# Kernel tuning notes

Measured on AMD Instinct MI355X. Metric: run time of the kernel, lower is better.

The kernel has to match this reference:

```python
import jax, jax.numpy as jnp
import numpy as np

C, N, D, DQ, K = 8, 16384, 1024, 128, 128  # clusters, patches/cluster, feat dim, q dim, top_k per cluster


def setup_inputs() -> dict:
    key = jax.random.key(0)
    ks = jax.random.split(key, 4)
    s = 0.02
    return {
        "cluster_features": jax.random.normal(ks[0], (C, N, D), jnp.float32),
        "key_feats": jax.random.normal(ks[1], (C, 1, D), jnp.float32),
        "Wq": jax.random.normal(ks[2], (D, DQ), jnp.float32) * s,
        "bq": jnp.zeros((DQ,), jnp.float32),
        "Wv": jax.random.normal(ks[3], (D, D), jnp.float32) * s,
        "bv": jnp.zeros((D,), jnp.float32),
    }


def _ranking_topk(feats, key_feat, Wq, bq, Wv, bv):
    # feats: [n, d], key_feat: [1, d]
    Q = feats @ Wq + bq                     # [n, DQ]
    qk = key_feat @ Wq + bq                 # [1, DQ]
    A = Q @ qk.T                            # [n, 1] attention scores
    A = jax.nn.softmax(A / jnp.sqrt(jnp.float32(DQ)), axis=0)
    top_vals, top_idx = jax.lax.top_k(A[:, 0], K)   # sorted descending, like torch.topk
    top_feats = feats[top_idx]              # [K, d] gather
    V = top_feats @ Wv + bv                 # value projection on gathered subset only
    A_ = jax.nn.softmax(top_vals[:, None] / jnp.sqrt(jnp.float32(D)), axis=0)  # [K, 1]
    fusion = (A_.T @ V)[0]                  # [d] fused weighted sum
    return top_feats, fusion


def reference(cluster_features, key_feats, Wq, bq, Wv, bv):
    top_feats, fusion = jax.vmap(
        lambda f, kf: _ranking_topk(f, kf, Wq, bq, Wv, bv)
    )(cluster_features, key_feats)
    # concat per-cluster selections; C*K == num_sample_feature so no padding branch
    selected_features = top_feats.reshape(C * K, D)
    cluster_fusion_feature = fusion         # [C, D]
    return selected_features, cluster_fusion_feature
```

## Files before the change

### kernel.cpp

```cpp
#include <hip/hip_runtime.h>

#define C_CLUST 8
#define N_PAT   16384
#define D_FEAT  1024
#define DQ_DIM  128
#define K_TOP   128

#define INV_S128 0.08838834764831844055
#define INV_S1024 0.03125

__device__ inline unsigned f2key(float f) {
    unsigned u = __float_as_uint(f);
    return (u & 0x80000000u) ? ~u : (u | 0x80000000u);
}
__device__ inline float key2f(unsigned k) {
    unsigned u = (k & 0x80000000u) ? (k ^ 0x80000000u) : ~k;
    return __uint_as_float(u);
}

__global__ __launch_bounds__(128) void qk_kernel(
    const float* __restrict__ key_feats,
    const float* __restrict__ Wq,
    double* __restrict__ qk_part)
{
    const int b = blockIdx.x;
    const int c = b >> 4, sg = b & 15;
    const int j = threadIdx.x;
    const int d0 = sg * 64;
    double acc = 0.0;
#pragma unroll 4
    for (int d = d0; d < d0 + 64; ++d)
        acc += (double)key_feats[c * D_FEAT + d] * (double)Wq[d * DQ_DIM + j];
    qk_part[(size_t)(c * 16 + sg) * DQ_DIM + j] = acc;
}

__global__ __launch_bounds__(256) void r_kernel(
    const float* __restrict__ Wq,
    const float* __restrict__ bq,
    const double* __restrict__ qk_part,
    double* __restrict__ r,
    double* __restrict__ b0)
{
    const int w = blockIdx.x * 4 + (threadIdx.x >> 6);
    const int lane = threadIdx.x & 63;
    const int c = w >> 10, d = w & (D_FEAT - 1);

    double q0 = (double)bq[lane];
    double q1 = (double)bq[64 + lane];
#pragma unroll
    for (int sg = 0; sg < 16; ++sg) {
        q0 += qk_part[(size_t)(c * 16 + sg) * DQ_DIM + lane];
        q1 += qk_part[(size_t)(c * 16 + sg) * DQ_DIM + 64 + lane];
    }

    double a = (double)Wq[d * DQ_DIM + lane] * q0
             + (double)Wq[d * DQ_DIM + 64 + lane] * q1;
#pragma unroll
    for (int o = 32; o > 0; o >>= 1) a += __shfl_xor(a, o, 64);
    if (lane == 0) r[c * D_FEAT + d] = a;

    if (d == 0) {
        double p = (double)bq[lane] * q0 + (double)bq[64 + lane] * q1;
#pragma unroll
        for (int o = 32; o > 0; o >>= 1) p += __shfl_xor(p, o, 64);
        if (lane == 0) b0[c] = p;
    }
}

__global__ __launch_bounds__(256) void score_kernel(
    const float* __restrict__ feats,
    const double* __restrict__ r,
    const double* __restrict__ b0,
    float* __restrict__ scores)
{
    const int w    = blockIdx.x * 4 + (threadIdx.x >> 6);
    const int lane = threadIdx.x & 63;
    const int c  = w >> 10;
    const int n0 = (w & 1023) * 16;

    const double* rp = r + c * D_FEAT;
    double rr[16];
#pragma unroll
    for (int it = 0; it < 4; ++it)
#pragma unroll
        for (int j = 0; j < 4; ++j)
            rr[it * 4 + j] = rp[it * 256 + lane * 4 + j];
    const double bb = b0[c];

    const float4* fbase = (const float4*)(feats + (size_t)(c * N_PAT + n0) * D_FEAT);
    float* sout = scores + c * N_PAT + n0;

    for (int rI = 0; rI < 16; rI += 2) {
        const float4* fp0 = fbase + (size_t)(rI + 0) * 256;
        const float4* fp1 = fbase + (size_t)(rI + 1) * 256;
        double acc0 = 0.0, acc1 = 0.0;
#pragma unroll
        for (int it = 0; it < 4; ++it) {
            float4 f0 = fp0[it * 64 + lane];
            float4 f1 = fp1[it * 64 + lane];
            acc0 += (double)f0.x * rr[it * 4 + 0];
            acc0 += (double)f0.y * rr[it * 4 + 1];
            acc0 += (double)f0.z * rr[it * 4 + 2];
            acc0 += (double)f0.w * rr[it * 4 + 3];
            acc1 += (double)f1.x * rr[it * 4 + 0];
            acc1 += (double)f1.y * rr[it * 4 + 1];
            acc1 += (double)f1.z * rr[it * 4 + 2];
            acc1 += (double)f1.w * rr[it * 4 + 3];
        }
#pragma unroll
        for (int o = 32; o > 0; o >>= 1) {
            acc0 += __shfl_xor(acc0, o, 64);
            acc1 += __shfl_xor(acc1, o, 64);
        }
        if (lane == 0) {
            sout[rI + 0] = (float)(acc0 + bb);
            sout[rI + 1] = (float)(acc1 + bb);
        }
    }
}

__global__ __launch_bounds__(1024) void topk_kernel(
    const float* __restrict__ scores,
    int* __restrict__ top_idx,
    double* __restrict__ Aw)
{
    const int c = blockIdx.x;
    const int tid = threadIdx.x;
    const int lane = tid & 63, wid = tid >> 6;

    __shared__ double   red_d[16];
    __shared__ unsigned red_u[16];
    __shared__ unsigned bcast_u;
    __shared__ double   bcast_d;
    __shared__ unsigned hist16[16][16];
    __shared__ unsigned total16[16];
    __shared__ unsigned bcast_b, bcast_need;
    __shared__ int cntG, cntE;
    __shared__ int idxG[K_TOP];
    __shared__ int idxE[256];
    __shared__ int list[K_TOP];
    __shared__ unsigned long long pairs[K_TOP];
    __shared__ double pd[K_TOP];
    __shared__ double red2[2];

    float sv[16];
    unsigned uk[16];
#pragma unroll
    for (int k = 0; k < 16; ++k) {
        sv[k] = scores[c * N_PAT + k * 1024 + tid];
        uk[k] = f2key(sv[k]);
    }

    unsigned mk = 0;
#pragma unroll
    for (int k = 0; k < 16; ++k) mk = max(mk, uk[k]);
#pragma unroll
    for (int o = 32; o > 0; o >>= 1) mk = max(mk, __shfl_xor(mk, o, 64));
    if (lane == 0) red_u[wid] = mk;
    __syncthreads();
    if (tid == 0) {
        unsigned m = 0;
        for (int i = 0; i < 16; ++i) m = max(m, red_u[i]);
        bcast_u = m;
    }
    __syncthreads();
    const double m_t = (double)key2f(bcast_u) * INV_S128;

    double zs = 0.0;
#pragma unroll
    for (int k = 0; k < 16; ++k)
        zs += (double)__expf((float)((double)sv[k] * INV_S128 - m_t));
#pragma unroll
    for (int o = 32; o > 0; o >>= 1) zs += __shfl_xor(zs, o, 64);
    if (lane == 0) red_d[wid] = zs;
    __syncthreads();
    if (tid == 0) {
        double z = 0.0;
        for (int i = 0; i < 16; ++i) z += red_d[i];
        bcast_d = z;
    }
    __syncthreads();
    const double Z = bcast_d;

    unsigned pref = 0;
    int need = K_TOP;
    for (int p = 7; p >= 0; --p) {
        const unsigned hmask = (p == 7) ? 0u : (0xFFFFFFFFu << (4 * (p + 1)));
        const unsigned b = (unsigned)lane & 15u;
        unsigned cnt = 0;
#pragma unroll
        for (int k = 0; k < 16; ++k) {
            bool act = (uk[k] & hmask) == pref;
            unsigned nib = (uk[k] >> (4 * p)) & 15u;
            unsigned long long mact = __ballot(act);
            unsigned long long m0 = __ballot((nib & 1u) != 0u);
            unsigned long long m1 = __ballot((nib & 2u) != 0u);
            unsigned long long m2 = __ballot((nib & 4u) != 0u);
            unsigned long long m3 = __ballot((nib & 8u) != 0u);
            unsigned long long sel = ((b & 1u) ? m0 : ~m0)
                                   & ((b & 2u) ? m1 : ~m1)
                                   & ((b & 4u) ? m2 : ~m2)
                                   & ((b & 8u) ? m3 : ~m3) & mact;
            cnt += (unsigned)__popcll(sel);
        }
        if (lane < 16) hist16[wid][lane] = cnt;
        __syncthreads();
        if (tid < 16) {
            unsigned t = 0;
#pragma unroll
            for (int wv2 = 0; wv2 < 16; ++wv2) t += hist16[wv2][tid];
            total16[tid] = t;
        }
        __syncthreads();
        if (tid < 16) {
            unsigned s = 0;
            for (int b2 = tid; b2 < 16; ++b2) s += total16[b2];
            unsigned hi = s - total16[tid];
            if (s >= (unsigned)need && hi < (unsigned)need) {
                bcast_b = (unsigned)tid;
                bcast_need = (unsigned)need - hi;
            }
        }
        __syncthreads();
        pref |= bcast_b << (4 * p);
        need = (int)bcast_need;
        __syncthreads();
    }
    const unsigned lo = pref;

    if (tid == 0) { cntG = 0; cntE = 0; }
    __syncthreads();
#pragma unroll
    for (int k = 0; k < 16; ++k) {
        int n = k * 1024 + tid;
        if (uk[k] > lo) {
            int p = atomicAdd(&cntG, 1);
            idxG[p] = n;
        } else if (uk[k] == lo) {
            int p = atomicAdd(&cntE, 1);
            if (p < 256) idxE[p] = n;
        }
    }
    __syncthreads();
    const int nG = cntG;
    const int nE = min(cntE, 256);
    if (tid == 0) {
        for (int i = 1; i < nE; ++i) {
            int v = idxE[i]; int j = i - 1;
            while (j >= 0 && idxE[j] > v) { idxE[j + 1] = idxE[j]; --j; }
            idxE[j + 1] = v;
        }
    }
    __syncthreads();
    if (tid < K_TOP) list[tid] = (tid < nG) ? idxG[tid] : idxE[tid - nG];
    __syncthreads();

    if (tid < K_TOP) {
        int idx = list[tid];
        unsigned key = f2key(scores[c * N_PAT + idx]);
        pairs[tid] = ((unsigned long long)key << 32) | (unsigned)(~(unsigned)idx);
    }
    for (int size = 2; size <= K_TOP; size <<= 1) {
        for (int stride = size >> 1; stride > 0; stride >>= 1) {
            __syncthreads();
            if (tid < K_TOP) {
                int p = tid ^ stride;
                if (p > tid) {
                    unsigned long long a = pairs[tid], b2 = pairs[p];
                    bool desc = ((tid & size) == 0);
                    if (desc ? (a < b2) : (a > b2)) { pairs[tid] = b2; pairs[p] = a; }
                }
            }
        }
    }
    __syncthreads();

    if (tid < K_TOP) {
        unsigned long long pr = pairs[tid];
        unsigned key = (unsigned)(pr >> 32);
        int idx = (int)(~(unsigned)(pr & 0xFFFFFFFFull));
        top_idx[c * K_TOP + tid] = idx;
        double s = (double)key2f(key);
        pd[tid] = exp(s * INV_S128 - m_t) / Z;
    }
    __syncthreads();
    if (tid < K_TOP) {
        double e = exp((pd[tid] - pd[0]) * INV_S1024);
        double se = e;
#pragma unroll
        for (int o = 32; o > 0; o >>= 1) se += __shfl_xor(se, o, 64);
        if (lane == 0) red2[wid] = se;
    }
    __syncthreads();
    if (tid < K_TOP) {
        double tot = red2[0] + red2[1];
        double e = exp((pd[tid] - pd[0]) * INV_S1024);
        Aw[c * K_TOP + tid] = e / tot;
    }
}

__global__ __launch_bounds__(256) void gather_wsum_kernel(
    const float* __restrict__ feats,
    const int* __restrict__ top_idx,
    const double* __restrict__ Aw,
    float* __restrict__ out,
    double* __restrict__ w_part)
{
    __shared__ double sa[32];
    __shared__ int sidx[32];
    const int b = blockIdx.x;
    const int c = b >> 4, quarter = (b >> 2) & 3, ich = b & 3;
    const int tid = threadIdx.x;
    if (tid < 32) {
        sa[tid] = Aw[c * K_TOP + ich * 32 + tid];
        sidx[tid] = top_idx[c * K_TOP + ich * 32 + tid];
    }
    __syncthreads();
    const int d = quarter * 256 + tid;
    const float* fc = feats + (size_t)c * N_PAT * D_FEAT + d;
    float* oc = out + ((size_t)c * K_TOP + ich * 32) * D_FEAT + d;
    double a0 = 0.0, a1 = 0.0, a2 = 0.0, a3 = 0.0;
#pragma unroll 2
    for (int i = 0; i < 32; i += 4) {
        float v0 = fc[(size_t)sidx[i + 0] * D_FEAT];
        float v1 = fc[(size_t)sidx[i + 1] * D_FEAT];
        float v2 = fc[(size_t)sidx[i + 2] * D_FEAT];
        float v3 = fc[(size_t)sidx[i + 3] * D_FEAT];
        oc[(size_t)(i + 0) * D_FEAT] = v0;
        oc[(size_t)(i + 1) * D_FEAT] = v1;
        oc[(size_t)(i + 2) * D_FEAT] = v2;
        oc[(size_t)(i + 3) * D_FEAT] = v3;
        a0 += sa[i + 0] * (double)v0;
        a1 += sa[i + 1] * (double)v1;
        a2 += sa[i + 2] * (double)v2;
        a3 += sa[i + 3] * (double)v3;
    }
    w_part[((size_t)(c * 4 + ich)) * D_FEAT + d] = (a0 + a1) + (a2 + a3);
}

__global__ __launch_bounds__(256) void fusion_kernel(
    const double* __restrict__ w_part,
    const float* __restrict__ Wv,
    const float* __restrict__ bv,
    float* __restrict__ out)
{
    __shared__ double w_lds[D_FEAT];
    __shared__ double partl[2][128];
    const int b = blockIdx.x;
    const int c = b >> 3, dpg = b & 7;
    const int tid = threadIdx.x;

    for (int d = tid; d < D_FEAT; d += 256) {
        double s = 0.0;
#pragma unroll
        for (int ich = 0; ich < 4; ++ich)
            s += w_part[((size_t)(c * 4 + ich)) * D_FEAT + d];
        w_lds[d] = s;
    }
    __syncthreads();

    const int dpl = tid & 127, half = tid >> 7;
    const int dp = dpg * 128 + dpl;
    const double* wc = w_lds + half * 512;
    const float* wvp = Wv + (size_t)(half * 512) * D_FEAT + dp;
    double a0 = 0.0, a1 = 0.0, a2 = 0.0, a3 = 0.0;
#pragma unroll 2
    for (int d = 0; d < 512; d += 4) {
        a0 += wc[d + 0] * (double)wvp[(size_t)(d + 0) * D_FEAT];
        a1 += wc[d + 1] * (double)wvp[(size_t)(d + 1) * D_FEAT];
        a2 += wc[d + 2] * (double)wvp[(size_t)(d + 2) * D_FEAT];
        a3 += wc[d + 3] * (double)wvp[(size_t)(d + 3) * D_FEAT];
    }
    partl[half][dpl] = (a0 + a1) + (a2 + a3);
    __syncthreads();
    if (half == 0) {
        double acc = (double)bv[dp] + partl[0][dpl] + partl[1][dpl];
        out[(size_t)(C_CLUST * K_TOP * D_FEAT) + c * D_FEAT + dp] = (float)acc;
    }
}

extern "C" void kernel_launch(void* const* d_in, const int* in_sizes, int n_in,
                              void* d_out, int out_size, void* d_ws, size_t ws_size,
                              hipStream_t stream) {
    const float* feats     = (const float*)d_in[0];
    const float* key_feats = (const float*)d_in[1];
    const float* Wq        = (const float*)d_in[2];
    const float* bq        = (const float*)d_in[3];
    const float* Wv        = (const float*)d_in[4];
    const float* bv        = (const float*)d_in[5];
    float* out = (float*)d_out;

    char* ws = (char*)d_ws;
    float*  scores  = (float*)(ws + 0);
    double* qk_part = (double*)(ws + 524288);
    double* r       = (double*)(ws + 655360);
    double* b0      = (double*)(ws + 720896);
    int*    top_idx = (int*)(ws + 720960);
    double* Aw      = (double*)(ws + 725056);
    double* w_part  = (double*)(ws + 733248);

    hipLaunchKernelGGL(qk_kernel,          dim3(C_CLUST * 16), dim3(128), 0, stream, key_feats, Wq, qk_part);
    hipLaunchKernelGGL(r_kernel,           dim3(2048),    dim3(256),  0, stream, Wq, bq, qk_part, r, b0);
    hipLaunchKernelGGL(score_kernel,       dim3(2048),    dim3(256),  0, stream, feats, r, b0, scores);
    hipLaunchKernelGGL(topk_kernel,        dim3(C_CLUST), dim3(1024), 0, stream, scores, top_idx, Aw);
    hipLaunchKernelGGL(gather_wsum_kernel, dim3(128),     dim3(256),  0, stream, feats, top_idx, Aw, out, w_part);
    hipLaunchKernelGGL(fusion_kernel,      dim3(64),      dim3(256),  0, stream, w_part, Wv, bv, out);
}
```

Before: 213.1 us.

## Fuse all stages into one cooperative kernel with grid syncs and hierarchical top-k

Replaces the six separate launches with one cooperative kernel of 512 blocks that runs the stages in order, separated by grid-wide barriers, removing the launch gaps between kernels. The single-block-per-cluster radix top-k is replaced by a two-level selection: 16 blocks per cluster each bitonic-sort a 1024-score chunk and keep their top 128 candidates, then one block per cluster merges the 2048 candidates. The softmax denominator is assembled from per-chunk maxima and sums. The risks are a fixed grid of 512 blocks doing the bandwidth-heavy score pass (64 rows per wave instead of 16), many idle blocks in the later stages, and the cost of the bitonic sorts in shared memory.

```diff
diff --git a/kernel.cpp b/kernel.cpp
--- a/kernel.cpp
+++ b/kernel.cpp
@@ -1,4 +1,7 @@
 #include <hip/hip_runtime.h>
+#include <hip/hip_cooperative_groups.h>
+
+namespace cg = cooperative_groups;
 
 #define C_CLUST 8
 #define N_PAT   16384
@@ -18,364 +21,290 @@
     return __uint_as_float(u);
 }
 
-__global__ __launch_bounds__(128) void qk_kernel(
+__global__ __launch_bounds__(256, 2) void mega_kernel(
+    const float* __restrict__ feats,
     const float* __restrict__ key_feats,
     const float* __restrict__ Wq,
-    double* __restrict__ qk_part)
-{
-    const int b = blockIdx.x;
-    const int c = b >> 4, sg = b & 15;
-    const int j = threadIdx.x;
-    const int d0 = sg * 64;
-    double acc = 0.0;
-#pragma unroll 4
-    for (int d = d0; d < d0 + 64; ++d)
-        acc += (double)key_feats[c * D_FEAT + d] * (double)Wq[d * DQ_DIM + j];
-    qk_part[(size_t)(c * 16 + sg) * DQ_DIM + j] = acc;
-}
-
-__global__ __launch_bounds__(256) void r_kernel(
-    const float* __restrict__ Wq,
     const float* __restrict__ bq,
-    const double* __restrict__ qk_part,
-    double* __restrict__ r,
-    double* __restrict__ b0)
-{
-    const int w = blockIdx.x * 4 + (threadIdx.x >> 6);
-    const int lane = threadIdx.x & 63;
-    const int c = w >> 10, d = w & (D_FEAT - 1);
-
-    double q0 = (double)bq[lane];
-    double q1 = (double)bq[64 + lane];
-#pragma unroll
-    for (int sg = 0; sg < 16; ++sg) {
-        q0 += qk_part[(size_t)(c * 16 + sg) * DQ_DIM + lane];
-        q1 += qk_part[(size_t)(c * 16 + sg) * DQ_DIM + 64 + lane];
-    }
-
-    double a = (double)Wq[d * DQ_DIM + lane] * q0
-             + (double)Wq[d * DQ_DIM + 64 + lane] * q1;
-#pragma unroll
-    for (int o = 32; o > 0; o >>= 1) a += __shfl_xor(a, o, 64);
-    if (lane == 0) r[c * D_FEAT + d] = a;
-
-    if (d == 0) {
-        double p = (double)bq[lane] * q0 + (double)bq[64 + lane] * q1;
-#pragma unroll
-        for (int o = 32; o > 0; o >>= 1) p += __shfl_xor(p, o, 64);
-        if (lane == 0) b0[c] = p;
-    }
-}
-
-__global__ __launch_bounds__(256) void score_kernel(
-    const float* __restrict__ feats,
-    const double* __restrict__ r,
-    const double* __restrict__ b0,
-    float* __restrict__ scores)
-{
-    const int w    = blockIdx.x * 4 + (threadIdx.x >> 6);
-    const int lane = threadIdx.x & 63;
-    const int c  = w >> 10;
-    const int n0 = (w & 1023) * 16;
-
-    const double* rp = r + c * D_FEAT;
-    double rr[16];
-#pragma unroll
-    for (int it = 0; it < 4; ++it)
-#pragma unroll
-        for (int j = 0; j < 4; ++j)
-            rr[it * 4 + j] = rp[it * 256 + lane * 4 + j];
-    const double bb = b0[c];
-
-    const float4* fbase = (const float4*)(feats + (size_t)(c * N_PAT + n0) * D_FEAT);
-    float* sout = scores + c * N_PAT + n0;
-
-    for (int rI = 0; rI < 16; rI += 2) {
-        const float4* fp0 = fbase + (size_t)(rI + 0) * 256;
-        const float4* fp1 = fbase + (size_t)(rI + 1) * 256;
-        double acc0 = 0.0, acc1 = 0.0;
-#pragma unroll
-        for (int it = 0; it < 4; ++it) {
-            float4 f0 = fp0[it * 64 + lane];
-            float4 f1 = fp1[it * 64 + lane];
-            acc0 += (double)f0.x * rr[it * 4 + 0];
-            acc0 += (double)f0.y * rr[it * 4 + 1];
-            acc0 += (double)f0.z * rr[it * 4 + 2];
-            acc0 += (double)f0.w * rr[it * 4 + 3];
-            acc1 += (double)f1.x * rr[it * 4 + 0];
-            acc1 += (double)f1.y * rr[it * 4 + 1];
-            acc1 += (double)f1.z * rr[it * 4 + 2];
-            acc1 += (double)f1.w * rr[it * 4 + 3];
-        }
-#pragma unroll
-        for (int o = 32; o > 0; o >>= 1) {
-            acc0 += __shfl_xor(acc0, o, 64);
-            acc1 += __shfl_xor(acc1, o, 64);
-        }
-        if (lane == 0) {
-            sout[rI + 0] = (float)(acc0 + bb);
-            sout[rI + 1] = (float)(acc1 + bb);
-        }
-    }
-}
-
-__global__ __launch_bounds__(1024) void topk_kernel(
-    const float* __restrict__ scores,
-    int* __restrict__ top_idx,
-    double* __restrict__ Aw)
-{
-    const int c = blockIdx.x;
-    const int tid = threadIdx.x;
-    const int lane = tid & 63, wid = tid >> 6;
-
-    __shared__ double   red_d[16];
-    __shared__ unsigned red_u[16];
-    __shared__ unsigned bcast_u;
-    __shared__ double   bcast_d;
-    __shared__ unsigned hist16[16][16];
-    __shared__ unsigned total16[16];
-    __shared__ unsigned bcast_b, bcast_need;
-    __shared__ int cntG, cntE;
-    __shared__ int idxG[K_TOP];
-    __shared__ int idxE[256];
-    __shared__ int list[K_TOP];
-    __shared__ unsigned long long pairs[K_TOP];
-    __shared__ double pd[K_TOP];
-    __shared__ double red2[2];
-
-    float sv[16];
-    unsigned uk[16];
-#pragma unroll
-    for (int k = 0; k < 16; ++k) {
-        sv[k] = scores[c * N_PAT + k * 1024 + tid];
-        uk[k] = f2key(sv[k]);
-    }
-
-    unsigned mk = 0;
-#pragma unroll
-    for (int k = 0; k < 16; ++k) mk = max(mk, uk[k]);
-#pragma unroll
-    for (int o = 32; o > 0; o >>= 1) mk = max(mk, __shfl_xor(mk, o, 64));
-    if (lane == 0) red_u[wid] = mk;
-    __syncthreads();
-    if (tid == 0) {
-        unsigned m = 0;
-        for (int i = 0; i < 16; ++i) m = max(m, red_u[i]);
-        bcast_u = m;
-    }
-    __syncthreads();
-    const double m_t = (double)key2f(bcast_u) * INV_S128;
-
-    double zs = 0.0;
-#pragma unroll
-    for (int k = 0; k < 16; ++k)
-        zs += (double)__expf((float)((double)sv[k] * INV_S128 - m_t));
-#pragma unroll
-    for (int o = 32; o > 0; o >>= 1) zs += __shfl_xor(zs, o, 64);
-    if (lane == 0) red_d[wid] = zs;
-    __syncthreads();
-    if (tid == 0) {
-        double z = 0.0;
-        for (int i = 0; i < 16; ++i) z += red_d[i];
-        bcast_d = z;
-    }
-    __syncthreads();
-    const double Z = bcast_d;
-
-    unsigned pref = 0;
-    int need = K_TOP;
-    for (int p = 7; p >= 0; --p) {
-        const unsigned hmask = (p == 7) ? 0u : (0xFFFFFFFFu << (4 * (p + 1)));
-        const unsigned b = (unsigned)lane & 15u;
-        unsigned cnt = 0;
-#pragma unroll
-        for (int k = 0; k < 16; ++k) {
-            bool act = (uk[k] & hmask) == pref;
-            unsigned nib = (uk[k] >> (4 * p)) & 15u;
-            unsigned long long mact = __ballot(act);
-            unsigned long long m0 = __ballot((nib & 1u) != 0u);
-            unsigned long long m1 = __ballot((nib & 2u) != 0u);
-            unsigned long long m2 = __ballot((nib & 4u) != 0u);
-            unsigned long long m3 = __ballot((nib & 8u) != 0u);
-            unsigned long long sel = ((b & 1u) ? m0 : ~m0)
-                                   & ((b & 2u) ? m1 : ~m1)
-                                   & ((b & 4u) ? m2 : ~m2)
-                                   & ((b & 8u) ? m3 : ~m3) & mact;
-            cnt += (unsigned)__popcll(sel);
-        }
-        if (lane < 16) hist16[wid][lane] = cnt;
-        __syncthreads();
-        if (tid < 16) {
-            unsigned t = 0;
-#pragma unroll
-            for (int wv2 = 0; wv2 < 16; ++wv2) t += hist16[wv2][tid];
-            total16[tid] = t;
-        }
-        __syncthreads();
-        if (tid < 16) {
-            unsigned s = 0;
-            for (int b2 = tid; b2 < 16; ++b2) s += total16[b2];
-            unsigned hi = s - total16[tid];
-            if (s >= (unsigned)need && hi < (unsigned)need) {
-                bcast_b = (unsigned)tid;
-                bcast_need = (unsigned)need - hi;
-            }
-        }
-        __syncthreads();
-        pref |= bcast_b << (4 * p);
-        need = (int)bcast_need;
-        __syncthreads();
-    }
-    const unsigned lo = pref;
-
-    if (tid == 0) { cntG = 0; cntE = 0; }
-    __syncthreads();
-#pragma unroll
-    for (int k = 0; k < 16; ++k) {
-        int n = k * 1024 + tid;
-        if (uk[k] > lo) {
-            int p = atomicAdd(&cntG, 1);
-            idxG[p] = n;
-        } else if (uk[k] == lo) {
-            int p = atomicAdd(&cntE, 1);
-            if (p < 256) idxE[p] = n;
-        }
-    }
-    __syncthreads();
-    const int nG = cntG;
-    const int nE = min(cntE, 256);
-    if (tid == 0) {
-        for (int i = 1; i < nE; ++i) {
-            int v = idxE[i]; int j = i - 1;
-            while (j >= 0 && idxE[j] > v) { idxE[j + 1] = idxE[j]; --j; }
-            idxE[j + 1] = v;
-        }
-    }
-    __syncthreads();
-    if (tid < K_TOP) list[tid] = (tid < nG) ? idxG[tid] : idxE[tid - nG];
-    __syncthreads();
-
-    if (tid < K_TOP) {
-        int idx = list[tid];
-        unsigned key = f2key(scores[c * N_PAT + idx]);
-        pairs[tid] = ((unsigned long long)key << 32) | (unsigned)(~(unsigned)idx);
-    }
-    for (int size = 2; size <= K_TOP; size <<= 1) {
-        for (int stride = size >> 1; stride > 0; stride >>= 1) {
-            __syncthreads();
-            if (tid < K_TOP) {
-                int p = tid ^ stride;
-                if (p > tid) {
-                    unsigned long long a = pairs[tid], b2 = pairs[p];
-                    bool desc = ((tid & size) == 0);
-                    if (desc ? (a < b2) : (a > b2)) { pairs[tid] = b2; pairs[p] = a; }
-                }
-            }
-        }
-    }
-    __syncthreads();
-
-    if (tid < K_TOP) {
-        unsigned long long pr = pairs[tid];
-        unsigned key = (unsigned)(pr >> 32);
-        int idx = (int)(~(unsigned)(pr & 0xFFFFFFFFull));
-        top_idx[c * K_TOP + tid] = idx;
-        double s = (double)key2f(key);
-        pd[tid] = exp(s * INV_S128 - m_t) / Z;
-    }
-    __syncthreads();
-    if (tid < K_TOP) {
-        double e = exp((pd[tid] - pd[0]) * INV_S1024);
-        double se = e;
-#pragma unroll
-        for (int o = 32; o > 0; o >>= 1) se += __shfl_xor(se, o, 64);
-        if (lane == 0) red2[wid] = se;
-    }
-    __syncthreads();
-    if (tid < K_TOP) {
-        double tot = red2[0] + red2[1];
-        double e = exp((pd[tid] - pd[0]) * INV_S1024);
-        Aw[c * K_TOP + tid] = e / tot;
-    }
-}
-
-__global__ __launch_bounds__(256) void gather_wsum_kernel(
-    const float* __restrict__ feats,
-    const int* __restrict__ top_idx,
-    const double* __restrict__ Aw,
-    float* __restrict__ out,
-    double* __restrict__ w_part)
-{
-    __shared__ double sa[32];
-    __shared__ int sidx[32];
-    const int b = blockIdx.x;
-    const int c = b >> 4, quarter = (b >> 2) & 3, ich = b & 3;
-    const int tid = threadIdx.x;
-    if (tid < 32) {
-        sa[tid] = Aw[c * K_TOP + ich * 32 + tid];
-        sidx[tid] = top_idx[c * K_TOP + ich * 32 + tid];
-    }
-    __syncthreads();
-    const int d = quarter * 256 + tid;
-    const float* fc = feats + (size_t)c * N_PAT * D_FEAT + d;
-    float* oc = out + ((size_t)c * K_TOP + ich * 32) * D_FEAT + d;
-    double a0 = 0.0, a1 = 0.0, a2 = 0.0, a3 = 0.0;
-#pragma unroll 2
-    for (int i = 0; i < 32; i += 4) {
-        float v0 = fc[(size_t)sidx[i + 0] * D_FEAT];
-        float v1 = fc[(size_t)sidx[i + 1] * D_FEAT];
-        float v2 = fc[(size_t)sidx[i + 2] * D_FEAT];
-        float v3 = fc[(size_t)sidx[i + 3] * D_FEAT];
-        oc[(size_t)(i + 0) * D_FEAT] = v0;
-        oc[(size_t)(i + 1) * D_FEAT] = v1;
-        oc[(size_t)(i + 2) * D_FEAT] = v2;
-        oc[(size_t)(i + 3) * D_FEAT] = v3;
-        a0 += sa[i + 0] * (double)v0;
-        a1 += sa[i + 1] * (double)v1;
-        a2 += sa[i + 2] * (double)v2;
-        a3 += sa[i + 3] * (double)v3;
-    }
-    w_part[((size_t)(c * 4 + ich)) * D_FEAT + d] = (a0 + a1) + (a2 + a3);
-}
-
-__global__ __launch_bounds__(256) void fusion_kernel(
-    const double* __restrict__ w_part,
     const float* __restrict__ Wv,
     const float* __restrict__ bv,
-    float* __restrict__ out)
+    float* __restrict__ out,
+    char* __restrict__ ws)
 {
-    __shared__ double w_lds[D_FEAT];
+    cg::grid_group grid = cg::this_grid();
+    const int b   = blockIdx.x;
+    const int tid = threadIdx.x;
+    const int lane = tid & 63, wvid = tid >> 6;
+
+    float*  scores  = (float*)(ws + 0);
+    double* qk_part = (double*)(ws + 524288);
+    double* r       = (double*)(ws + 655360);
+    double* b0      = (double*)(ws + 720896);
+    int*    top_idx = (int*)(ws + 720960);
+    double* Aw      = (double*)(ws + 725056);
+    double* w_part  = (double*)(ws + 733248);
+    unsigned long long* cand = (unsigned long long*)(ws + 995392);
+    unsigned* mxkey = (unsigned*)(ws + 1126464);
+    double*   Ssum  = (double*)(ws + 1126976);
+
+    __shared__ unsigned long long su[2048];
+    __shared__ double sdbl[D_FEAT];
     __shared__ double partl[2][128];
-    const int b = blockIdx.x;
-    const int c = b >> 3, dpg = b & 7;
-    const int tid = threadIdx.x;
-
-    for (int d = tid; d < D_FEAT; d += 256) {
-        double s = 0.0;
-#pragma unroll
-        for (int ich = 0; ich < 4; ++ich)
-            s += w_part[((size_t)(c * 4 + ich)) * D_FEAT + d];
-        w_lds[d] = s;
-    }
-    __syncthreads();
-
-    const int dpl = tid & 127, half = tid >> 7;
-    const int dp = dpg * 128 + dpl;
-    const double* wc = w_lds + half * 512;
-    const float* wvp = Wv + (size_t)(half * 512) * D_FEAT + dp;
-    double a0 = 0.0, a1 = 0.0, a2 = 0.0, a3 = 0.0;
+    __shared__ unsigned sred_u[4];
+    __shared__ double sred_d[4];
+    __shared__ double sZ;
+    __shared__ double sa_g[32];
+    __shared__ int sidx_g[32];
+
+    if (b < 128 && tid < 128) {
+        const int c = b >> 4, sg = b & 15;
+        const int d0 = sg * 64;
+        double acc = 0.0;
+#pragma unroll 4
+        for (int d = d0; d < d0 + 64; ++d)
+            acc += (double)key_feats[c * D_FEAT + d] * (double)Wq[d * DQ_DIM + tid];
+        qk_part[(size_t)(c * 16 + sg) * DQ_DIM + tid] = acc;
+    }
+    grid.sync();
+
+    {
+        const int gw = b * 4 + wvid;
+        const int c = gw >> 8;
+        double q0 = (double)bq[lane], q1 = (double)bq[64 + lane];
+#pragma unroll
+        for (int sg = 0; sg < 16; ++sg) {
+            q0 += qk_part[(size_t)(c * 16 + sg) * DQ_DIM + lane];
+            q1 += qk_part[(size_t)(c * 16 + sg) * DQ_DIM + 64 + lane];
+        }
+#pragma unroll
+        for (int t = 0; t < 4; ++t) {
+            const int d = (gw & 255) * 4 + t;
+            double a = (double)Wq[d * DQ_DIM + lane] * q0
+                     + (double)Wq[d * DQ_DIM + 64 + lane] * q1;
+#pragma unroll
+            for (int o = 32; o > 0; o >>= 1) a += __shfl_xor(a, o, 64);
+            if (lane == 0) r[c * D_FEAT + d] = a;
+        }
+        if ((gw & 255) == 0) {
+            double p = (double)bq[lane] * q0 + (double)bq[64 + lane] * q1;
+#pragma unroll
+            for (int o = 32; o > 0; o >>= 1) p += __shfl_xor(p, o, 64);
+            if (lane == 0) b0[c] = p;
+        }
+    }
+    grid.sync();
+
+    {
+        const int gw = b * 4 + wvid;
+        const int c = gw >> 8;
+        const int n0 = (gw & 255) * 64;
+        const double* rp = r + c * D_FEAT;
+        double rr[16];
+#pragma unroll
+        for (int it = 0; it < 4; ++it)
+#pragma unroll
+            for (int j = 0; j < 4; ++j)
+                rr[it * 4 + j] = rp[it * 256 + lane * 4 + j];
+        const double bb = b0[c];
+        const float4* fbase = (const float4*)(feats + (size_t)(c * N_PAT + n0) * D_FEAT);
+        float* sout = scores + c * N_PAT + n0;
+
+        for (int rI = 0; rI < 64; rI += 2) {
+            const float4* fp0 = fbase + (size_t)(rI + 0) * 256;
+            const float4* fp1 = fbase + (size_t)(rI + 1) * 256;
+            double acc0 = 0.0, acc1 = 0.0;
+#pragma unroll
+            for (int it = 0; it < 4; ++it) {
+                float4 f0 = fp0[it * 64 + lane];
+                float4 f1 = fp1[it * 64 + lane];
+                acc0 += (double)f0.x * rr[it * 4 + 0];
+                acc0 += (double)f0.y * rr[it * 4 + 1];
+                acc0 += (double)f0.z * rr[it * 4 + 2];
+                acc0 += (double)f0.w * rr[it * 4 + 3];
+                acc1 += (double)f1.x * rr[it * 4 + 0];
+                acc1 += (double)f1.y * rr[it * 4 + 1];
+                acc1 += (double)f1.z * rr[it * 4 + 2];
+                acc1 += (double)f1.w * rr[it * 4 + 3];
+            }
+#pragma unroll
+            for (int o = 32; o > 0; o >>= 1) {
+                acc0 += __shfl_xor(acc0, o, 64);
+                acc1 += __shfl_xor(acc1, o, 64);
+            }
+            if (lane == 0) {
+                sout[rI + 0] = (float)(acc0 + bb);
+                sout[rI + 1] = (float)(acc1 + bb);
+            }
+        }
+    }
+    grid.sync();
+
+    if (b < 128) {
+        const int c = b >> 4, chunk = b & 15;
+        const int sbase = c * N_PAT + chunk * 1024;
+        float sv[4];
+        unsigned kmax = 0;
+#pragma unroll
+        for (int q = 0; q < 4; ++q) {
+            const int li = q * 256 + tid;
+            float s = scores[sbase + li];
+            sv[q] = s;
+            unsigned key = f2key(s);
+            su[li] = ((unsigned long long)key << 32) | (unsigned)(~(unsigned)(chunk * 1024 + li));
+            kmax = max(kmax, key);
+        }
+#pragma unroll
+        for (int o = 32; o > 0; o >>= 1) kmax = max(kmax, __shfl_xor(kmax, o, 64));
+        if (lane == 0) sred_u[wvid] = kmax;
+        __syncthreads();
+        kmax = max(max(sred_u[0], sred_u[1]), max(sred_u[2], sred_u[3]));
+        const double mx_t = (double)key2f(kmax) * INV_S128;
+        double es = 0.0;
+#pragma unroll
+        for (int q = 0; q < 4; ++q)
+            es += (double)__expf((float)((double)sv[q] * INV_S128 - mx_t));
+#pragma unroll
+        for (int o = 32; o > 0; o >>= 1) es += __shfl_xor(es, o, 64);
+        if (lane == 0) sred_d[wvid] = es;
+        __syncthreads();
+        if (tid == 0) {
+            mxkey[c * 16 + chunk] = kmax;
+            Ssum[c * 16 + chunk] = sred_d[0] + sred_d[1] + sred_d[2] + sred_d[3];
+        }
+        for (int k = 2; k <= 1024; k <<= 1) {
+            for (int j = k >> 1; j > 0; j >>= 1) {
+                __syncthreads();
+                for (int i = tid; i < 1024; i += 256) {
+                    int l = i ^ j;
+                    if (l > i) {
+                        unsigned long long a = su[i], bb2 = su[l];
+                        bool desc = ((i & k) == 0);
+                        if (desc ? (a < bb2) : (a > bb2)) { su[i] = bb2; su[l] = a; }
+                    }
+                }
+            }
+        }
+        __syncthreads();
+        if (tid < 128) cand[(size_t)(c * 16 + chunk) * 128 + tid] = su[tid];
+    }
+    grid.sync();
+
+    if (b < 8) {
+        const int c = b;
+        for (int i = tid; i < 2048; i += 256) su[i] = cand[(size_t)c * 2048 + i];
+        __syncthreads();
+        for (int k = 2; k <= 2048; k <<= 1) {
+            for (int j = k >> 1; j > 0; j >>= 1) {
+                __syncthreads();
+                for (int i = tid; i < 2048; i += 256) {
+                    int l = i ^ j;
+                    if (l > i) {
+                        unsigned long long a = su[i], bb2 = su[l];
+                        bool desc = ((i & k) == 0);
+                        if (desc ? (a < bb2) : (a > bb2)) { su[i] = bb2; su[l] = a; }
+                    }
+                }
+            }
+        }
+        __syncthreads();
+
+        const unsigned mkey = (unsigned)(su[0] >> 32);
+        const double m_t = (double)key2f(mkey) * INV_S128;
+        double z = 0.0;
+        if (tid < 16)
+            z = Ssum[c * 16 + tid] *
+                exp((double)key2f(mxkey[c * 16 + tid]) * INV_S128 - m_t);
+        if (wvid == 0) {
+#pragma unroll
+            for (int o = 32; o > 0; o >>= 1) z += __shfl_xor(z, o, 64);
+            if (tid == 0) sZ = z;
+        }
+        __syncthreads();
+        const double Z = sZ;
+
+        double* pd = (double*)partl;
+        if (tid < K_TOP) {
+            unsigned long long pr = su[tid];
+            top_idx[c * K_TOP + tid] = (int)(~(unsigned)(pr & 0xFFFFFFFFull));
+            double s = (double)key2f((unsigned)(pr >> 32));
+            pd[tid] = exp(s * INV_S128 - m_t) / Z;
+        }
+        __syncthreads();
+        if (tid < K_TOP) {
+            double e = exp((pd[tid] - pd[0]) * INV_S1024);
+            double se = e;
+#pragma unroll
+            for (int o = 32; o > 0; o >>= 1) se += __shfl_xor(se, o, 64);
+            if (lane == 0) sred_d[wvid] = se;
+        }
+        __syncthreads();
+        if (tid < K_TOP) {
+            double tot = sred_d[0] + sred_d[1];
+            double e = exp((pd[tid] - pd[0]) * INV_S1024);
+            Aw[c * K_TOP + tid] = e / tot;
+        }
+    }
+    grid.sync();
+
+    if (b < 128) {
+        const int c = b >> 4, quarter = (b >> 2) & 3, ich = b & 3;
+        if (tid < 32) {
+            sa_g[tid] = Aw[c * K_TOP + ich * 32 + tid];
+            sidx_g[tid] = top_idx[c * K_TOP + ich * 32 + tid];
+        }
+        __syncthreads();
+        const int d = quarter * 256 + tid;
+        const float* fc = feats + (size_t)c * N_PAT * D_FEAT + d;
+        float* oc = out + ((size_t)c * K_TOP + ich * 32) * D_FEAT + d;
+        double a0 = 0.0, a1 = 0.0, a2 = 0.0, a3 = 0.0;
 #pragma unroll 2
-    for (int d = 0; d < 512; d += 4) {
-        a0 += wc[d + 0] * (double)wvp[(size_t)(d + 0) * D_FEAT];
-        a1 += wc[d + 1] * (double)wvp[(size_t)(d + 1) * D_FEAT];
-        a2 += wc[d + 2] * (double)wvp[(size_t)(d + 2) * D_FEAT];
-        a3 += wc[d + 3] * (double)wvp[(size_t)(d + 3) * D_FEAT];
-    }
-    partl[half][dpl] = (a0 + a1) + (a2 + a3);
-    __syncthreads();
-    if (half == 0) {
-        double acc = (double)bv[dp] + partl[0][dpl] + partl[1][dpl];
-        out[(size_t)(C_CLUST * K_TOP * D_FEAT) + c * D_FEAT + dp] = (float)acc;
+        for (int i = 0; i < 32; i += 4) {
+            float v0 = fc[(size_t)sidx_g[i + 0] * D_FEAT];
+            float v1 = fc[(size_t)sidx_g[i + 1] * D_FEAT];
+            float v2 = fc[(size_t)sidx_g[i + 2] * D_FEAT];
+            float v3 = fc[(size_t)sidx_g[i + 3] * D_FEAT];
+            oc[(size_t)(i + 0) * D_FEAT] = v0;
+            oc[(size_t)(i + 1) * D_FEAT] = v1;
+            oc[(size_t)(i + 2) * D_FEAT] = v2;
+            oc[(size_t)(i + 3) * D_FEAT] = v3;
+            double aw0 = sa_g[i + 0], aw1 = sa_g[i + 1], aw2 = sa_g[i + 2], aw3 = sa_g[i + 3];
+            a0 += aw0 * (double)v0;
+            a1 += aw1 * (double)v1;
+            a2 += aw2 * (double)v2;
+            a3 += aw3 * (double)v3;
+        }
+        w_part[((size_t)(c * 4 + ich)) * D_FEAT + d] = (a0 + a1) + (a2 + a3);
+    }
+    grid.sync();
+
+    if (b < 64) {
+        const int c = b >> 3, dpg = b & 7;
+        for (int d = tid; d < D_FEAT; d += 256) {
+            double s = 0.0;
+#pragma unroll
+            for (int ich = 0; ich < 4; ++ich)
+                s += w_part[((size_t)(c * 4 + ich)) * D_FEAT + d];
+            sdbl[d] = s;
+        }
+        __syncthreads();
+        const int dpl = tid & 127, half = tid >> 7;
+        const int dp = dpg * 128 + dpl;
+        const double* wc = sdbl + half * 512;
+        const float* wvp = Wv + (size_t)(half * 512) * D_FEAT + dp;
+        double a0 = 0.0, a1 = 0.0, a2 = 0.0, a3 = 0.0;
+#pragma unroll 2
+        for (int d = 0; d < 512; d += 4) {
+            a0 += wc[d + 0] * (double)wvp[(size_t)(d + 0) * D_FEAT];
+            a1 += wc[d + 1] * (double)wvp[(size_t)(d + 1) * D_FEAT];
+            a2 += wc[d + 2] * (double)wvp[(size_t)(d + 2) * D_FEAT];
+            a3 += wc[d + 3] * (double)wvp[(size_t)(d + 3) * D_FEAT];
+        }
+        partl[half][dpl] = (a0 + a1) + (a2 + a3);
+        __syncthreads();
+        if (half == 0) {
+            double acc = (double)bv[dp] + partl[0][dpl] + partl[1][dpl];
+            out[(size_t)(C_CLUST * K_TOP * D_FEAT) + c * D_FEAT + dp] = (float)acc;
+        }
     }
 }
 
@@ -389,20 +318,12 @@
     const float* Wv        = (const float*)d_in[4];
     const float* bv        = (const float*)d_in[5];
     float* out = (float*)d_out;
-
     char* ws = (char*)d_ws;
-    float*  scores  = (float*)(ws + 0);
-    double* qk_part = (double*)(ws + 524288);
-    double* r       = (double*)(ws + 655360);
-    double* b0      = (double*)(ws + 720896);
-    int*    top_idx = (int*)(ws + 720960);
-    double* Aw      = (double*)(ws + 725056);
-    double* w_part  = (double*)(ws + 733248);
-
-    hipLaunchKernelGGL(qk_kernel,          dim3(C_CLUST * 16), dim3(128), 0, stream, key_feats, Wq, qk_part);
-    hipLaunchKernelGGL(r_kernel,           dim3(2048),    dim3(256),  0, stream, Wq, bq, qk_part, r, b0);
-    hipLaunchKernelGGL(score_kernel,       dim3(2048),    dim3(256),  0, stream, feats, r, b0, scores);
-    hipLaunchKernelGGL(topk_kernel,        dim3(C_CLUST), dim3(1024), 0, stream, scores, top_idx, Aw);
-    hipLaunchKernelGGL(gather_wsum_kernel, dim3(128),     dim3(256),  0, stream, feats, top_idx, Aw, out, w_part);
-    hipLaunchKernelGGL(fusion_kernel,      dim3(64),      dim3(256),  0, stream, w_part, Wv, bv, out);
+
+    void* args[] = {
+        (void*)&feats, (void*)&key_feats, (void*)&Wq, (void*)&bq,
+        (void*)&Wv, (void*)&bv, (void*)&out, (void*)&ws
+    };
+    hipLaunchCooperativeKernel((const void*)mega_kernel,
+                               dim3(512), dim3(256), args, 0, stream);
 }
```

New measurement: 557.4 us. 162% more time.

## Fuse qk and r prep kernels; use wave-level sort and scan in top-k

Applied to the files above, without the earlier changes.

Merges the two small projection kernels (qk partials and r vector) into one prep kernel that reduces key@Wq in LDS and then computes r, removing a launch and a global round trip. In the top-k kernel the histogram prefix scan now runs inside a single wave with shuffles, which drops one barrier per radix pass. The 128-element bitonic sort moves from shared memory with block barriers to register shuffles inside one wave. The cost is that each prep block recomputes the full qk vector for its cluster (8x redundant), and the sort now runs on one wave only.

```diff
diff --git a/kernel.cpp b/kernel.cpp
--- a/kernel.cpp
+++ b/kernel.cpp
@@ -17,53 +17,66 @@
     unsigned u = (k & 0x80000000u) ? (k ^ 0x80000000u) : ~k;
     return __uint_as_float(u);
 }
-
-__global__ __launch_bounds__(128) void qk_kernel(
+__device__ inline unsigned long long shfl_xor_u64(unsigned long long v, int m) {
+    unsigned lo = (unsigned)v, hi = (unsigned)(v >> 32);
+    lo = __shfl_xor(lo, m, 64);
+    hi = __shfl_xor(hi, m, 64);
+    return ((unsigned long long)hi << 32) | lo;
+}
+
+__global__ __launch_bounds__(1024) void prep_kernel(
     const float* __restrict__ key_feats,
     const float* __restrict__ Wq,
-    double* __restrict__ qk_part)
-{
-    const int b = blockIdx.x;
-    const int c = b >> 4, sg = b & 15;
-    const int j = threadIdx.x;
-    const int d0 = sg * 64;
-    double acc = 0.0;
-#pragma unroll 4
-    for (int d = d0; d < d0 + 64; ++d)
-        acc += (double)key_feats[c * D_FEAT + d] * (double)Wq[d * DQ_DIM + j];
-    qk_part[(size_t)(c * 16 + sg) * DQ_DIM + j] = acc;
-}
-
-__global__ __launch_bounds__(256) void r_kernel(
-    const float* __restrict__ Wq,
     const float* __restrict__ bq,
-    const double* __restrict__ qk_part,
     double* __restrict__ r,
     double* __restrict__ b0)
 {
-    const int w = blockIdx.x * 4 + (threadIdx.x >> 6);
-    const int lane = threadIdx.x & 63;
-    const int c = w >> 10, d = w & (D_FEAT - 1);
-
-    double q0 = (double)bq[lane];
-    double q1 = (double)bq[64 + lane];
-#pragma unroll
-    for (int sg = 0; sg < 16; ++sg) {
-        q0 += qk_part[(size_t)(c * 16 + sg) * DQ_DIM + lane];
-        q1 += qk_part[(size_t)(c * 16 + sg) * DQ_DIM + 64 + lane];
-    }
-
-    double a = (double)Wq[d * DQ_DIM + lane] * q0
-             + (double)Wq[d * DQ_DIM + 64 + lane] * q1;
-#pragma unroll
-    for (int o = 32; o > 0; o >>= 1) a += __shfl_xor(a, o, 64);
-    if (lane == 0) r[c * D_FEAT + d] = a;
-
-    if (d == 0) {
-        double p = (double)bq[lane] * q0 + (double)bq[64 + lane] * q1;
+    __shared__ float keyrow[D_FEAT];
+    __shared__ double part[1024];
+    __shared__ double qk_lds[DQ_DIM];
+    const int b = blockIdx.x;
+    const int c = b >> 3, g = b & 7;
+    const int tid = threadIdx.x;
+    const int lane = tid & 63, wv = tid >> 6;
+
+    keyrow[tid] = key_feats[c * D_FEAT + tid];
+    __syncthreads();
+
+    {
+        const int j = tid & 127, s = tid >> 7;
+        double acc = 0.0;
+        for (int d = s; d < D_FEAT; d += 8)
+            acc += (double)keyrow[d] * (double)Wq[d * DQ_DIM + j];
+        part[s * DQ_DIM + j] = acc;
+    }
+    __syncthreads();
+    if (tid < DQ_DIM) {
+        double v = part[tid];
+#pragma unroll
+        for (int s2 = 1; s2 < 8; ++s2) v += part[s2 * DQ_DIM + tid];
+        qk_lds[tid] = v + (double)bq[tid];
+    }
+    __syncthreads();
+
+    if (g == 0 && wv == 0) {
+        double p = (double)bq[lane] * qk_lds[lane] + (double)bq[64 + lane] * qk_lds[64 + lane];
 #pragma unroll
         for (int o = 32; o > 0; o >>= 1) p += __shfl_xor(p, o, 64);
         if (lane == 0) b0[c] = p;
+    }
+
+    {
+        const double q0 = qk_lds[lane], q1 = qk_lds[64 + lane];
+        const int d0 = g * 128 + wv * 8;
+#pragma unroll
+        for (int i = 0; i < 8; ++i) {
+            const int d = d0 + i;
+            double a = (double)Wq[d * DQ_DIM + lane] * q0
+                     + (double)Wq[d * DQ_DIM + 64 + lane] * q1;
+#pragma unroll
+            for (int o = 32; o > 0; o >>= 1) a += __shfl_xor(a, o, 64);
+            if (lane == 0) r[c * D_FEAT + d] = a;
+        }
     }
 }
 
@@ -133,15 +146,11 @@
     __shared__ unsigned bcast_u;
     __shared__ double   bcast_d;
     __shared__ unsigned hist16[16][16];
-    __shared__ unsigned total16[16];
     __shared__ unsigned bcast_b, bcast_need;
     __shared__ int cntG, cntE;
     __shared__ int idxG[K_TOP];
     __shared__ int idxE[256];
     __shared__ int list[K_TOP];
-    __shared__ unsigned long long pairs[K_TOP];
-    __shared__ double pd[K_TOP];
-    __shared__ double red2[2];
 
     float sv[16];
     unsigned uk[16];
@@ -186,7 +195,7 @@
     int need = K_TOP;
     for (int p = 7; p >= 0; --p) {
         const unsigned hmask = (p == 7) ? 0u : (0xFFFFFFFFu << (4 * (p + 1)));
-        const unsigned b = (unsigned)lane & 15u;
+        const unsigned bkt = (unsigned)lane & 15u;
         unsigned cnt = 0;
 #pragma unroll
         for (int k = 0; k < 16; ++k) {
@@ -197,34 +206,37 @@
             unsigned long long m1 = __ballot((nib & 2u) != 0u);
             unsigned long long m2 = __ballot((nib & 4u) != 0u);
             unsigned long long m3 = __ballot((nib & 8u) != 0u);
-            unsigned long long sel = ((b & 1u) ? m0 : ~m0)
-                                   & ((b & 2u) ? m1 : ~m1)
-                                   & ((b & 4u) ? m2 : ~m2)
-                                   & ((b & 8u) ? m3 : ~m3) & mact;
+            unsigned long long sel = ((bkt & 1u) ? m0 : ~m0)
+                                   & ((bkt & 2u) ? m1 : ~m1)
+                                   & ((bkt & 4u) ? m2 : ~m2)
+                                   & ((bkt & 8u) ? m3 : ~m3) & mact;
             cnt += (unsigned)__popcll(sel);
         }
         if (lane < 16) hist16[wid][lane] = cnt;
         __syncthreads();
-        if (tid < 16) {
+        if (wid == 0) {
             unsigned t = 0;
-#pragma unroll
-            for (int wv2 = 0; wv2 < 16; ++wv2) t += hist16[wv2][tid];
-            total16[tid] = t;
-        }
-        __syncthreads();
-        if (tid < 16) {
-            unsigned s = 0;
-            for (int b2 = tid; b2 < 16; ++b2) s += total16[b2];
-            unsigned hi = s - total16[tid];
-            if (s >= (unsigned)need && hi < (unsigned)need) {
-                bcast_b = (unsigned)tid;
-                bcast_need = (unsigned)need - hi;
+            if (lane < 16) {
+#pragma unroll
+                for (int w2 = 0; w2 < 16; ++w2) t += hist16[w2][lane];
+            }
+            unsigned s = t;
+#pragma unroll
+            for (int off = 1; off < 16; off <<= 1) {
+                unsigned o = __shfl_down(s, off, 64);
+                if (lane + off < 16) s += o;
+            }
+            if (lane < 16) {
+                unsigned hi = s - t;
+                if (s >= (unsigned)need && hi < (unsigned)need) {
+                    bcast_b = (unsigned)lane;
+                    bcast_need = (unsigned)need - hi;
+                }
             }
         }
         __syncthreads();
         pref |= bcast_b << (4 * p);
         need = (int)bcast_need;
-        __syncthreads();
     }
     const unsigned lo = pref;
 
@@ -255,47 +267,49 @@
     if (tid < K_TOP) list[tid] = (tid < nG) ? idxG[tid] : idxE[tid - nG];
     __syncthreads();
 
-    if (tid < K_TOP) {
-        int idx = list[tid];
-        unsigned key = f2key(scores[c * N_PAT + idx]);
-        pairs[tid] = ((unsigned long long)key << 32) | (unsigned)(~(unsigned)idx);
-    }
-    for (int size = 2; size <= K_TOP; size <<= 1) {
-        for (int stride = size >> 1; stride > 0; stride >>= 1) {
-            __syncthreads();
-            if (tid < K_TOP) {
-                int p = tid ^ stride;
-                if (p > tid) {
-                    unsigned long long a = pairs[tid], b2 = pairs[p];
-                    bool desc = ((tid & size) == 0);
-                    if (desc ? (a < b2) : (a > b2)) { pairs[tid] = b2; pairs[p] = a; }
-                }
+    if (wid == 0) {
+        const int idxA = list[lane], idxB = list[lane + 64];
+        unsigned long long v0 = ((unsigned long long)f2key(scores[c * N_PAT + idxA]) << 32)
+                              | (unsigned)(~(unsigned)idxA);
+        unsigned long long v1 = ((unsigned long long)f2key(scores[c * N_PAT + idxB]) << 32)
+                              | (unsigned)(~(unsigned)idxB);
+        for (int k = 2; k <= 64; k <<= 1) {
+            for (int j = k >> 1; j > 0; j >>= 1) {
+                const bool d0 = (k == 64) ? true  : ((lane & k) == 0);
+                const bool d1 = (k == 64) ? false : d0;
+                const bool lower = ((lane & j) == 0);
+                unsigned long long o0 = shfl_xor_u64(v0, j);
+                unsigned long long o1 = shfl_xor_u64(v1, j);
+                v0 = (lower == d0) ? (v0 > o0 ? v0 : o0) : (v0 < o0 ? v0 : o0);
+                v1 = (lower == d1) ? (v1 > o1 ? v1 : o1) : (v1 < o1 ? v1 : o1);
             }
         }
-    }
-    __syncthreads();
-
-    if (tid < K_TOP) {
-        unsigned long long pr = pairs[tid];
-        unsigned key = (unsigned)(pr >> 32);
-        int idx = (int)(~(unsigned)(pr & 0xFFFFFFFFull));
-        top_idx[c * K_TOP + tid] = idx;
-        double s = (double)key2f(key);
-        pd[tid] = exp(s * INV_S128 - m_t) / Z;
-    }
-    __syncthreads();
-    if (tid < K_TOP) {
-        double e = exp((pd[tid] - pd[0]) * INV_S1024);
-        double se = e;
-#pragma unroll
-        for (int o = 32; o > 0; o >>= 1) se += __shfl_xor(se, o, 64);
-        if (lane == 0) red2[wid] = se;
-    }
-    __syncthreads();
-    if (tid < K_TOP) {
-        double tot = red2[0] + red2[1];
-        double e = exp((pd[tid] - pd[0]) * INV_S1024);
-        Aw[c * K_TOP + tid] = e / tot;
+        {
+            unsigned long long hi = v0 > v1 ? v0 : v1;
+            unsigned long long lo2 = v0 > v1 ? v1 : v0;
+            v0 = hi; v1 = lo2;
+        }
+        for (int j = 32; j > 0; j >>= 1) {
+            const bool lower = ((lane & j) == 0);
+            unsigned long long o0 = shfl_xor_u64(v0, j);
+            unsigned long long o1 = shfl_xor_u64(v1, j);
+            v0 = lower ? (v0 > o0 ? v0 : o0) : (v0 < o0 ? v0 : o0);
+            v1 = lower ? (v1 > o1 ? v1 : o1) : (v1 < o1 ? v1 : o1);
+        }
+        const int oidx0 = (int)(~(unsigned)(v0 & 0xFFFFFFFFull));
+        const int oidx1 = (int)(~(unsigned)(v1 & 0xFFFFFFFFull));
+        top_idx[c * K_TOP + lane]      = oidx0;
+        top_idx[c * K_TOP + 64 + lane] = oidx1;
+        const double p0 = exp((double)key2f((unsigned)(v0 >> 32)) * INV_S128 - m_t) / Z;
+        const double p1 = exp((double)key2f((unsigned)(v1 >> 32)) * INV_S128 - m_t) / Z;
+        const double pmax = __shfl(p0, 0, 64);
+        const double e0 = exp((p0 - pmax) * INV_S1024);
+        const double e1 = exp((p1 - pmax) * INV_S1024);
+        double tot = e0 + e1;
+#pragma unroll
+        for (int o = 32; o > 0; o >>= 1) tot += __shfl_xor(tot, o, 64);
+        Aw[c * K_TOP + lane]      = e0 / tot;
+        Aw[c * K_TOP + 64 + lane] = e1 / tot;
     }
 }
 
@@ -392,17 +406,20 @@
 
     char* ws = (char*)d_ws;
     float*  scores  = (float*)(ws + 0);
-    double* qk_part = (double*)(ws + 524288);
-    double* r       = (double*)(ws + 655360);
-    double* b0      = (double*)(ws + 720896);
-    int*    top_idx = (int*)(ws + 720960);
-    double* Aw      = (double*)(ws + 725056);
-    double* w_part  = (double*)(ws + 733248);
-
-    hipLaunchKernelGGL(qk_kernel,          dim3(C_CLUST * 16), dim3(128), 0, stream, key_feats, Wq, qk_part);
-    hipLaunchKernelGGL(r_kernel,           dim3(2048),    dim3(256),  0, stream, Wq, bq, qk_part, r, b0);
-    hipLaunchKernelGGL(score_kernel,       dim3(2048),    dim3(256),  0, stream, feats, r, b0, scores);
-    hipLaunchKernelGGL(topk_kernel,        dim3(C_CLUST), dim3(1024), 0, stream, scores, top_idx, Aw);
-    hipLaunchKernelGGL(gather_wsum_kernel, dim3(128),     dim3(256),  0, stream, feats, top_idx, Aw, out, w_part);
-    hipLaunchKernelGGL(fusion_kernel,      dim3(64),      dim3(256),  0, stream, w_part, Wv, bv, out);
-}
+    double* r       = (double*)(ws + 524288);
+    double* b0      = (double*)(ws + 589824);
+    int*    top_idx = (int*)(ws + 589888);
+    double* Aw      = (double*)(ws + 593984);
+    double* w_part  = (double*)(ws + 602176);
+
+    hipLaunchKernelGGL(prep_kernel,        dim3(64),   dim3(1024), 0, stream,
+                       key_feats, Wq, bq, r, b0);
+    hipLaunchKernelGGL(score_kernel,       dim3(2048), dim3(256),  0, stream,
+                       feats, r, b0, scores);
+    hipLaunchKernelGGL(topk_kernel,        dim3(C_CLUST), dim3(1024), 0, stream,
+                       scores, top_idx, Aw);
+    hipLaunchKernelGGL(gather_wsum_kernel, dim3(128),  dim3(256),  0, stream,
+                       feats, top_idx, Aw, out, w_part);
+    hipLaunchKernelGGL(fusion_kernel,      dim3(64),   dim3(256),  0, stream,
+                       w_part, Wv, bv, out);
+}
```

Result: slower. 244.4 us (+14.7%).
